# Kernel optimization log

Hardware: AMD Instinct MI355X
Metric: run time of the kernel (lower is better)

The kernel has to match this reference:

```python
import jax, jax.numpy as jnp
import numpy as np

N, E, F, H, C, G = 50000, 600000, 128, 128, 10, 500
NUM_GIN = 3
BN_EPS = 1e-5


def _bn(x, gamma, beta):
    # BatchNorm1d in training mode: batch statistics over node/graph dim
    m = jnp.mean(x, axis=0)
    v = jnp.mean((x - m) ** 2, axis=0)
    return (x - m) * jax.lax.rsqrt(v + BN_EPS) * gamma + beta


def setup_inputs() -> dict:
    key = jax.random.key(0)
    ks = jax.random.split(key, 16)
    s = 1.0 / np.sqrt(H)
    inp = {
        "x": jax.random.normal(ks[0], (N, F), dtype=jnp.float32),
        "edge_index": jax.random.randint(ks[1], (2, E), 0, N),
        "batch": jnp.sort(jax.random.randint(ks[2], (N,), 0, G)),
        # bn_feat
        "gamma_feat": jnp.ones((F,), jnp.float32),
        "beta_feat": jnp.full((F,), 1e-4, jnp.float32),
        # conv_feat (GCNConv gfn=True -> pure linear)
        "W_feat": jax.random.uniform(ks[3], (F, H), jnp.float32, -s, s),
        "b_feat": jnp.zeros((H,), jnp.float32),
        # GIN conv MLPs, stacked over 3 layers
        "gin_W1": jax.random.uniform(ks[4], (NUM_GIN, H, H), jnp.float32, -s, s),
        "gin_b1": jnp.zeros((NUM_GIN, H), jnp.float32),
        "gin_gamma": jnp.ones((NUM_GIN, H), jnp.float32),
        "gin_beta": jnp.full((NUM_GIN, H), 1e-4, jnp.float32),
        "gin_W2": jax.random.uniform(ks[5], (NUM_GIN, H, H), jnp.float32, -s, s),
        "gin_b2": jnp.zeros((NUM_GIN, H), jnp.float32),
        # one FC block (num_fc_layers=2 -> 1 bn+lin)
        "gamma_fc": jnp.ones((H,), jnp.float32),
        "beta_fc": jnp.full((H,), 1e-4, jnp.float32),
        "W_fc": jax.random.uniform(ks[6], (H, H), jnp.float32, -s, s),
        "b_fc": jnp.zeros((H,), jnp.float32),
        # bn_hidden + classifier
        "gamma_h": jnp.ones((H,), jnp.float32),
        "beta_h": jnp.full((H,), 1e-4, jnp.float32),
        "W_cls": jax.random.uniform(ks[7], (H, C), jnp.float32, -s, s),
        "b_cls": jnp.zeros((C,), jnp.float32),
    }
    return inp


def reference(x, gamma_feat, beta_feat, W_feat, b_feat,
              gin_W1, gin_b1, gin_gamma, gin_beta, gin_W2, gin_b2,
              gamma_fc, beta_fc, W_fc, b_fc,
              gamma_h, beta_h, W_cls, b_cls,
              edge_index, batch):
    src, dst = edge_index[0], edge_index[1]
    h = _bn(x, gamma_feat, beta_feat)
    h = jax.nn.relu(h @ W_feat + b_feat)  # GCNConv gfn=True == Linear
    for i in range(NUM_GIN):
        # GIN aggregation: (1+eps)*x + sum_{j->i} x_j, eps=0
        agg = jnp.zeros_like(h).at[dst].add(h[src])
        z = h + agg
        z = jax.nn.relu(_bn(z @ gin_W1[i] + gin_b1[i], gin_gamma[i], gin_beta[i]))
        h = jax.nn.relu(z @ gin_W2[i] + gin_b2[i])
    g = jax.ops.segment_sum(h, batch, num_segments=G)  # global_add_pool -> [G,H]
    g = jax.nn.relu(_bn(g, gamma_fc, beta_fc) @ W_fc + b_fc)
    g = _bn(g, gamma_h, beta_h)
    logits = g @ W_cls + b_cls
    return jax.nn.log_softmax(logits, axis=-1)
```

## Files before the change

kernel.cpp:

```cpp
#include <hip/hip_runtime.h>
#include <math.h>

#define N_NODES 50000
#define N_EDGES 600000
#define HDIM 128
#define NCLS 10
#define NGRAPH 500
#define BN_EPS 1e-5f
#define SCAN_BLOCKS 196

__global__ void colstats_kernel(const float* __restrict__ X, int M, float* __restrict__ stats) {
    int col = threadIdx.x & 127;
    int sub = threadIdx.x >> 7;
    float s = 0.f, sq = 0.f;
    for (int r = blockIdx.x * 2 + sub; r < M; r += gridDim.x * 2) {
        float v = X[(size_t)r * HDIM + col];
        s += v; sq += v * v;
    }
    atomicAdd(&stats[col], s);
    atomicAdd(&stats[HDIM + col], sq);
}

__global__ void hist_kernel(const int* __restrict__ ei, int* __restrict__ counts) {
    int e = blockIdx.x * 256 + threadIdx.x;
    if (e < N_EDGES) atomicAdd(&counts[ei[N_EDGES + e]], 1);
}

__global__ __launch_bounds__(256) void scan1_kernel(const int* __restrict__ counts,
                                                    int* __restrict__ partial,
                                                    int* __restrict__ blockSums) {
    __shared__ int tmp[256];
    int tid = threadIdx.x;
    int i = blockIdx.x * 256 + tid;
    int v = (i < N_NODES) ? counts[i] : 0;
    tmp[tid] = v;
    __syncthreads();
#pragma unroll
    for (int off = 1; off < 256; off <<= 1) {
        int t = (tid >= off) ? tmp[tid - off] : 0;
        __syncthreads();
        tmp[tid] += t;
        __syncthreads();
    }
    if (i < N_NODES) partial[i] = tmp[tid] - v;
    if (tid == 255) blockSums[blockIdx.x] = tmp[255];
}

__global__ __launch_bounds__(256) void scan2_kernel(const int* __restrict__ blockSums,
                                                    int* __restrict__ blockBase) {
    __shared__ int tmp[256];
    int tid = threadIdx.x;
    int v = (tid < SCAN_BLOCKS) ? blockSums[tid] : 0;
    tmp[tid] = v;
    __syncthreads();
#pragma unroll
    for (int off = 1; off < 256; off <<= 1) {
        int t = (tid >= off) ? tmp[tid - off] : 0;
        __syncthreads();
        tmp[tid] += t;
        __syncthreads();
    }
    if (tid < SCAN_BLOCKS) blockBase[tid] = tmp[tid] - v;
}

__global__ __launch_bounds__(256) void scan3_kernel(const int* __restrict__ partial,
                                                    const int* __restrict__ blockBase,
                                                    int* __restrict__ offsets,
                                                    int* __restrict__ cursor) {
    int i = blockIdx.x * 256 + threadIdx.x;
    if (i < N_NODES) {
        int o = partial[i] + blockBase[blockIdx.x];
        offsets[i] = o;
        cursor[i] = o;
    }
    if (i == 0) offsets[N_NODES] = N_EDGES;
}

__global__ void fill_kernel(const int* __restrict__ ei, int* __restrict__ cursor, int* __restrict__ csr) {
    int e = blockIdx.x * 256 + threadIdx.x;
    if (e < N_EDGES) {
        int d = ei[N_EDGES + e];
        int pos = atomicAdd(&cursor[d], 1);
        csr[pos] = ei[e];
    }
}

__global__ __launch_bounds__(256) void agg_kernel(const float* __restrict__ h,
                                                  const int* __restrict__ offsets,
                                                  const int* __restrict__ csr,
                                                  float* __restrict__ z) {
    int node = (blockIdx.x * 256 + threadIdx.x) >> 6;
    int lane = threadIdx.x & 63;
    if (node >= N_NODES) return;
    int c0 = lane * 2;
    int beg = offsets[node], end = offsets[node + 1];
    const float2 self = *(const float2*)&h[(size_t)node * HDIM + c0];
    float ax = self.x, ay = self.y;
    for (int j = beg; j < end; j += 64) {
        int cnt = min(64, end - j);
        int sl = (j + lane < end) ? csr[j + lane] : 0;
        int t = 0;
        for (; t + 4 <= cnt; t += 4) {
            int s0 = __shfl(sl, t, 64);
            int s1 = __shfl(sl, t + 1, 64);
            int s2 = __shfl(sl, t + 2, 64);
            int s3 = __shfl(sl, t + 3, 64);
            float2 v0 = *(const float2*)&h[(size_t)s0 * HDIM + c0];
            float2 v1 = *(const float2*)&h[(size_t)s1 * HDIM + c0];
            float2 v2 = *(const float2*)&h[(size_t)s2 * HDIM + c0];
            float2 v3 = *(const float2*)&h[(size_t)s3 * HDIM + c0];
            ax += v0.x + v1.x + v2.x + v3.x;
            ay += v0.y + v1.y + v2.y + v3.y;
        }
        for (; t < cnt; t++) {
            int s = __shfl(sl, t, 64);
            float2 hv = *(const float2*)&h[(size_t)s * HDIM + c0];
            ax += hv.x; ay += hv.y;
        }
    }
    float2 o; o.x = ax; o.y = ay;
    *(float2*)&z[(size_t)node * HDIM + c0] = o;
}

__global__ __launch_bounds__(128) void segsum2_kernel(const float* __restrict__ h,
                                                      const int* __restrict__ batch,
                                                      float* __restrict__ g) {
    int b = blockIdx.x;
    int tid = threadIdx.x;
    __shared__ int bounds[2];
    if (tid < 2) {
        int target = b + tid;
        int lo = 0, hi = N_NODES;
        while (lo < hi) {
            int mid = (lo + hi) >> 1;
            if (batch[mid] < target) lo = mid + 1; else hi = mid;
        }
        bounds[tid] = lo;
    }
    __syncthreads();
    int beg = bounds[0], end = bounds[1];
    float s = 0.f;
    for (int r = beg; r < end; r++) s += h[(size_t)r * HDIM + tid];
    g[b * HDIM + tid] = s;
}

template <bool PRE_A, bool PRE_B, bool RELU, bool STATS>
__global__ __launch_bounds__(256, 3) void gemm_bn(const float* A, const float* __restrict__ B,
                                                  const float* __restrict__ bias, float* C, int M,
                                                  const float* __restrict__ statsPre,
                                                  const float* __restrict__ gammaPre,
                                                  const float* __restrict__ betaPre,
                                                  float invCnt, float* __restrict__ statsOut) {
    __shared__ float At[64][65];
    __shared__ float Bs[64][128];
    __shared__ float aPre[128], bPre[128];

    const int tid = threadIdx.x;
    const int tx = tid & 15, ty = tid >> 4;
    const int r0 = blockIdx.x * 64;

    if (PRE_A || PRE_B) {
        if (tid < 128) {
            float m = statsPre[tid] * invCnt;
            float v = statsPre[128 + tid] * invCnt - m * m;
            float a = gammaPre[tid] * rsqrtf(v + BN_EPS);
            aPre[tid] = a;
            bPre[tid] = betaPre[tid] - m * a;
        }
        __syncthreads();
    }

    float acc[4][8];
#pragma unroll
    for (int i = 0; i < 4; i++)
#pragma unroll
        for (int j = 0; j < 8; j++) acc[i][j] = 0.f;

    float biasEff[8];
#pragma unroll
    for (int j = 0; j < 8; j++) biasEff[j] = bias[8 * tx + j];
    if (PRE_B) {
        for (int k = 0; k < 128; k++) {
            float bb = bPre[k];
            const float* Brow = B + (size_t)k * HDIM + 8 * tx;
#pragma unroll
            for (int j = 0; j < 8; j++) biasEff[j] = fmaf(bb, Brow[j], biasEff[j]);
        }
    }

    for (int kc = 0; kc < 128; kc += 64) {
#pragma unroll
        for (int i = 0; i < 4; i++) {
            int f4 = tid + i * 256;
            int row = f4 >> 4;
            int kg = f4 & 15;
            int grow = r0 + row;
            float4 av;
            if (grow < M) av = *(const float4*)(A + (size_t)grow * HDIM + kc + kg * 4);
            else av = make_float4(0.f, 0.f, 0.f, 0.f);
            if (PRE_A) {
                int kb = kc + kg * 4;
                av.x = fmaxf(fmaf(av.x, aPre[kb + 0], bPre[kb + 0]), 0.f);
                av.y = fmaxf(fmaf(av.y, aPre[kb + 1], bPre[kb + 1]), 0.f);
                av.z = fmaxf(fmaf(av.z, aPre[kb + 2], bPre[kb + 2]), 0.f);
                av.w = fmaxf(fmaf(av.w, aPre[kb + 3], bPre[kb + 3]), 0.f);
            }
            At[kg * 4 + 0][row] = av.x;
            At[kg * 4 + 1][row] = av.y;
            At[kg * 4 + 2][row] = av.z;
            At[kg * 4 + 3][row] = av.w;
        }
#pragma unroll
        for (int i = 0; i < 8; i++) {
            int f4 = tid + i * 256;
            int krow = f4 >> 5;
            int cg = f4 & 31;
            float4 bv = *(const float4*)(B + (size_t)(kc + krow) * HDIM + cg * 4);
            if (PRE_B) {
                float s = aPre[kc + krow];
                bv.x *= s; bv.y *= s; bv.z *= s; bv.w *= s;
            }
            *(float4*)&Bs[krow][cg * 4] = bv;
        }
        __syncthreads();
#pragma unroll 8
        for (int k = 0; k < 64; k++) {
            float av[4];
            av[0] = At[k][ty];
            av[1] = At[k][ty + 16];
            av[2] = At[k][ty + 32];
            av[3] = At[k][ty + 48];
            const float4 b0 = *(const float4*)&Bs[k][8 * tx];
            const float4 b1 = *(const float4*)&Bs[k][8 * tx + 4];
            float bv[8] = {b0.x, b0.y, b0.z, b0.w, b1.x, b1.y, b1.z, b1.w};
#pragma unroll
            for (int i = 0; i < 4; i++)
#pragma unroll
                for (int j = 0; j < 8; j++) acc[i][j] = fmaf(av[i], bv[j], acc[i][j]);
        }
        __syncthreads();
    }

    float s[8], sq[8];
    if (STATS) {
#pragma unroll
        for (int j = 0; j < 8; j++) { s[j] = 0.f; sq[j] = 0.f; }
    }
#pragma unroll
    for (int i = 0; i < 4; i++) {
        int grow = r0 + ty + 16 * i;
        if (grow < M) {
            float v[8];
#pragma unroll
            for (int j = 0; j < 8; j++) {
                v[j] = acc[i][j] + biasEff[j];
                if (RELU) v[j] = fmaxf(v[j], 0.f);
                if (STATS) { s[j] += v[j]; sq[j] += v[j] * v[j]; }
            }
            float4 o0 = make_float4(v[0], v[1], v[2], v[3]);
            float4 o1 = make_float4(v[4], v[5], v[6], v[7]);
            *(float4*)(C + (size_t)grow * HDIM + 8 * tx) = o0;
            *(float4*)(C + (size_t)grow * HDIM + 8 * tx + 4) = o1;
        }
    }
    if (STATS) {
        float* red = &At[0][0];
#pragma unroll
        for (int j = 0; j < 8; j++) {
            red[ty * 128 + 8 * tx + j] = s[j];
            red[2048 + ty * 128 + 8 * tx + j] = sq[j];
        }
        __syncthreads();
        if (tid < 128) {
            float t = 0.f;
#pragma unroll
            for (int u = 0; u < 16; u++) t += red[u * 128 + tid];
            atomicAdd(&statsOut[tid], t);
        } else {
            int col = tid - 128;
            float t = 0.f;
#pragma unroll
            for (int u = 0; u < 16; u++) t += red[2048 + u * 128 + col];
            atomicAdd(&statsOut[128 + col], t);
        }
    }
}

__global__ __launch_bounds__(256) void head_kernel(const float* __restrict__ g2,
                                                   const float* __restrict__ stats,
                                                   const float* __restrict__ gamma,
                                                   const float* __restrict__ beta,
                                                   const float* __restrict__ Wc,
                                                   const float* __restrict__ bc,
                                                   float* __restrict__ out, float invCnt) {
    __shared__ float Wf[HDIM * NCLS];
    __shared__ float bf[NCLS];
    __shared__ float aP[HDIM], bP[HDIM];
    const int tid = threadIdx.x;
    if (tid < HDIM) {
        float m = stats[tid] * invCnt;
        float v = stats[HDIM + tid] * invCnt - m * m;
        float a = gamma[tid] * rsqrtf(v + BN_EPS);
        aP[tid] = a;
        bP[tid] = beta[tid] - m * a;
    }
    __syncthreads();
    for (int idx = tid; idx < HDIM * NCLS; idx += 256) {
        int k = idx / NCLS;
        Wf[idx] = aP[k] * Wc[idx];
    }
    if (tid < NCLS) {
        float sv = bc[tid];
        for (int k = 0; k < HDIM; k++) sv = fmaf(bP[k], Wc[k * NCLS + tid], sv);
        bf[tid] = sv;
    }
    __syncthreads();
    int row = blockIdx.x * 256 + tid;
    if (row >= NGRAPH) return;
    float l[NCLS];
#pragma unroll
    for (int c = 0; c < NCLS; c++) l[c] = bf[c];
    for (int k = 0; k < HDIM; k++) {
        float gv = g2[row * HDIM + k];
#pragma unroll
        for (int c = 0; c < NCLS; c++) l[c] = fmaf(gv, Wf[k * NCLS + c], l[c]);
    }
    float mx = l[0];
#pragma unroll
    for (int c = 1; c < NCLS; c++) mx = fmaxf(mx, l[c]);
    float se = 0.f;
#pragma unroll
    for (int c = 0; c < NCLS; c++) se += expf(l[c] - mx);
    float lse = mx + logf(se);
#pragma unroll
    for (int c = 0; c < NCLS; c++) out[row * NCLS + c] = l[c] - lse;
}

extern "C" void kernel_launch(void* const* d_in, const int* in_sizes, int n_in,
                              void* d_out, int out_size, void* d_ws, size_t ws_size,
                              hipStream_t stream) {
    const float* x          = (const float*)d_in[0];
    const int*   ei         = (const int*)d_in[1];
    const int*   batch      = (const int*)d_in[2];
    const float* gamma_feat = (const float*)d_in[3];
    const float* beta_feat  = (const float*)d_in[4];
    const float* W_feat     = (const float*)d_in[5];
    const float* b_feat     = (const float*)d_in[6];
    const float* gin_W1     = (const float*)d_in[7];
    const float* gin_b1     = (const float*)d_in[8];
    const float* gin_gamma  = (const float*)d_in[9];
    const float* gin_beta   = (const float*)d_in[10];
    const float* gin_W2     = (const float*)d_in[11];
    const float* gin_b2     = (const float*)d_in[12];
    const float* gamma_fc   = (const float*)d_in[13];
    const float* beta_fc    = (const float*)d_in[14];
    const float* W_fc       = (const float*)d_in[15];
    const float* b_fc       = (const float*)d_in[16];
    const float* gamma_h    = (const float*)d_in[17];
    const float* beta_h     = (const float*)d_in[18];
    const float* W_cls      = (const float*)d_in[19];
    const float* b_cls      = (const float*)d_in[20];
    float* out = (float*)d_out;

    float* ws = (float*)d_ws;
    size_t off = 0;
    float* h  = ws + off; off += (size_t)N_NODES * HDIM;
    float* zy = ws + off; off += (size_t)N_NODES * HDIM;
    float* g2 = ws + off; off += NGRAPH * HDIM;
    float* g  = ws + off; off += NGRAPH * HDIM;
    size_t zstart = off;
    float* stats = ws + off; off += 256 * 6;
    int* counts = (int*)(ws + off); off += N_NODES;
    size_t zbytes = (off - zstart) * sizeof(float);
    int* offsets   = (int*)(ws + off); off += N_NODES + 1;
    int* cursor    = (int*)(ws + off); off += N_NODES;
    int* csr       = (int*)(ws + off); off += N_EDGES;
    int* partial   = (int*)(ws + off); off += N_NODES;
    int* blockSums = (int*)(ws + off); off += 256;
    int* blockBase = (int*)(ws + off); off += 256;

    float* statsX  = stats;
    float* statsY0 = stats + 256;
    float* statsY1 = stats + 512;
    float* statsY2 = stats + 768;
    float* statsYa[3] = {statsY0, statsY1, statsY2};
    float* statsG  = stats + 1024;
    float* statsG2 = stats + 1280;

    hipMemsetAsync(stats, 0, zbytes, stream);

    const float invN = 1.f / (float)N_NODES;
    const float invG = 1.f / (float)NGRAPH;
    const int gblocks = (N_NODES + 63) / 64;
    const int eblocks = (N_EDGES + 255) / 256;
    const int nwaves  = (N_NODES * 64 + 255) / 256;

    colstats_kernel<<<256, 256, 0, stream>>>(x, N_NODES, statsX);
    hist_kernel<<<eblocks, 256, 0, stream>>>(ei, counts);
    scan1_kernel<<<SCAN_BLOCKS, 256, 0, stream>>>(counts, partial, blockSums);
    scan2_kernel<<<1, 256, 0, stream>>>(blockSums, blockBase);
    scan3_kernel<<<SCAN_BLOCKS, 256, 0, stream>>>(partial, blockBase, offsets, cursor);
    fill_kernel<<<eblocks, 256, 0, stream>>>(ei, cursor, csr);

    gemm_bn<false, true, true, false><<<gblocks, 256, 0, stream>>>(
        x, W_feat, b_feat, h, N_NODES, statsX, gamma_feat, beta_feat, invN, nullptr);

    for (int i = 0; i < 3; i++) {
        agg_kernel<<<nwaves, 256, 0, stream>>>(h, offsets, csr, zy);
        gemm_bn<false, false, false, true><<<gblocks, 256, 0, stream>>>(
            zy, gin_W1 + i * HDIM * HDIM, gin_b1 + i * HDIM, zy, N_NODES,
            nullptr, nullptr, nullptr, invN, statsYa[i]);
        gemm_bn<true, false, true, false><<<gblocks, 256, 0, stream>>>(
            zy, gin_W2 + i * HDIM * HDIM, gin_b2 + i * HDIM, h, N_NODES,
            statsYa[i], gin_gamma + i * HDIM, gin_beta + i * HDIM, invN, nullptr);
    }

    segsum2_kernel<<<NGRAPH, 128, 0, stream>>>(h, batch, g);
    colstats_kernel<<<8, 256, 0, stream>>>(g, NGRAPH, statsG);
    gemm_bn<false, true, true, true><<<(NGRAPH + 63) / 64, 256, 0, stream>>>(
        g, W_fc, b_fc, g2, NGRAPH, statsG, gamma_fc, beta_fc, invG, statsG2);
    head_kernel<<<2, 256, 0, stream>>>(g2, statsG2, gamma_h, beta_h, W_cls, b_cls, out, invG);
}
```

Measured before the change: 737.4 us.

## Move node GEMMs to bf16x3 split-precision MFMA with pretransposed weights

Replaces the FP32 shared-memory GEMM kernels for the feature layer and the six GIN linear layers with an MFMA kernel. Each fp32 operand is split into a bf16 high part and a bf16 low part, and three bf16 MFMA products are summed to stay close to fp32 accuracy. Weights are split and transposed once by small prep kernels. The feature-layer batch norm is folded into the weights and bias, and the GIN batch norm plus ReLU is applied while loading A. This is meant to move the matmul work from SIMT FP32 onto the matrix cores, in exchange for extra split arithmetic and direct global loads of A and B with no LDS tiling.

```diff
diff --git a/kernel.cpp b/kernel.cpp
--- a/kernel.cpp
+++ b/kernel.cpp
@@ -8,6 +8,9 @@
 #define NGRAPH 500
 #define BN_EPS 1e-5f
 #define SCAN_BLOCKS 196
+
+typedef short bf16x8 __attribute__((ext_vector_type(8)));
+typedef float f32x4 __attribute__((ext_vector_type(4)));
 
 __global__ void colstats_kernel(const float* __restrict__ X, int M, float* __restrict__ stats) {
     int col = threadIdx.x & 127;
@@ -144,6 +147,176 @@
     g[b * HDIM + tid] = s;
 }
 
+__device__ inline void dekker_split(float v, unsigned short& hi, unsigned short& lo) {
+    unsigned u = __float_as_uint(v);
+    hi = (unsigned short)(u >> 16);
+    float flo = v - __uint_as_float(u & 0xffff0000u);
+    lo = (unsigned short)(__float_as_uint(flo) >> 16);
+}
+
+__global__ __launch_bounds__(256) void prep_w(const float* __restrict__ W1,
+                                              const float* __restrict__ W2,
+                                              unsigned short* __restrict__ wh,
+                                              unsigned short* __restrict__ wl) {
+    int m = blockIdx.x;
+    const float* src = (m < 3) ? (W1 + m * HDIM * HDIM) : (W2 + (m - 3) * HDIM * HDIM);
+    unsigned short* dh = wh + m * HDIM * HDIM;
+    unsigned short* dl = wl + m * HDIM * HDIM;
+    for (int i = threadIdx.x; i < HDIM * HDIM; i += 256) {
+        int n = i >> 7, k = i & 127;
+        float v = src[k * HDIM + n];
+        unsigned short h16, l16;
+        dekker_split(v, h16, l16);
+        dh[i] = h16; dl[i] = l16;
+    }
+}
+
+__global__ __launch_bounds__(256) void prep_feat(const float* __restrict__ W,
+                                                 const float* __restrict__ bfeat,
+                                                 const float* __restrict__ stats,
+                                                 const float* __restrict__ gamma,
+                                                 const float* __restrict__ beta,
+                                                 float invCnt,
+                                                 unsigned short* __restrict__ dh,
+                                                 unsigned short* __restrict__ dl,
+                                                 float* __restrict__ biasF) {
+    __shared__ float aP[HDIM], bP[HDIM];
+    int tid = threadIdx.x;
+    if (tid < HDIM) {
+        float m = stats[tid] * invCnt;
+        float v = stats[HDIM + tid] * invCnt - m * m;
+        float a = gamma[tid] * rsqrtf(v + BN_EPS);
+        aP[tid] = a;
+        bP[tid] = beta[tid] - m * a;
+    }
+    __syncthreads();
+    for (int i = tid; i < HDIM * HDIM; i += 256) {
+        int n = i >> 7, k = i & 127;
+        float v = aP[k] * W[k * HDIM + n];
+        unsigned short h16, l16;
+        dekker_split(v, h16, l16);
+        dh[i] = h16; dl[i] = l16;
+    }
+    if (tid < HDIM) {
+        float acc = bfeat[tid];
+        for (int k = 0; k < HDIM; k++) acc = fmaf(bP[k], W[k * HDIM + tid], acc);
+        biasF[tid] = acc;
+    }
+}
+
+template <int MODE>
+__global__ __launch_bounds__(256, 2) void mfma_gemm(const float* __restrict__ A,
+                                                    const unsigned short* __restrict__ Bh,
+                                                    const unsigned short* __restrict__ Bl,
+                                                    const float* __restrict__ bias,
+                                                    float* __restrict__ C, int M,
+                                                    const float* __restrict__ statsPre,
+                                                    const float* __restrict__ gammaPre,
+                                                    const float* __restrict__ betaPre,
+                                                    float invCnt,
+                                                    float* __restrict__ statsOut) {
+    const int tid = threadIdx.x;
+    const int w = tid >> 6, l = tid & 63;
+    const int q = l >> 4, c16 = l & 15;
+    const int rb = blockIdx.x * 128 + w * 32;
+
+    int rowA[2];
+#pragma unroll
+    for (int rt = 0; rt < 2; rt++) rowA[rt] = min(rb + rt * 16 + c16, M - 1);
+
+    float bs[8];
+#pragma unroll
+    for (int c = 0; c < 8; c++) bs[c] = bias[c * 16 + c16];
+
+    f32x4 acc[2][8];
+#pragma unroll
+    for (int rt = 0; rt < 2; rt++)
+#pragma unroll
+        for (int c = 0; c < 8; c++) acc[rt][c] = (f32x4){0.f, 0.f, 0.f, 0.f};
+
+#pragma unroll
+    for (int s = 0; s < 4; s++) {
+        const int k0 = s * 32 + q * 8;
+        float aK[8], bK[8];
+        if (MODE == 2) {
+#pragma unroll
+            for (int j = 0; j < 8; j++) {
+                int k = k0 + j;
+                float m = statsPre[k] * invCnt;
+                float var = statsPre[HDIM + k] * invCnt - m * m;
+                float a = gammaPre[k] * rsqrtf(var + BN_EPS);
+                aK[j] = a;
+                bK[j] = betaPre[k] - m * a;
+            }
+        }
+        bf16x8 ah[2], al[2];
+#pragma unroll
+        for (int rt = 0; rt < 2; rt++) {
+            const float* ap = A + (size_t)rowA[rt] * HDIM + k0;
+            float4 v0 = *(const float4*)ap;
+            float4 v1 = *(const float4*)(ap + 4);
+            float vv[8] = {v0.x, v0.y, v0.z, v0.w, v1.x, v1.y, v1.z, v1.w};
+#pragma unroll
+            for (int j = 0; j < 8; j++) {
+                float v = vv[j];
+                if (MODE == 2) v = fmaxf(fmaf(v, aK[j], bK[j]), 0.f);
+                unsigned u = __float_as_uint(v);
+                ah[rt][j] = (short)(u >> 16);
+                float flo = v - __uint_as_float(u & 0xffff0000u);
+                al[rt][j] = (short)(__float_as_uint(flo) >> 16);
+            }
+        }
+#pragma unroll
+        for (int c = 0; c < 8; c++) {
+            const size_t bo = (size_t)(c * 16 + c16) * HDIM + k0;
+            bf16x8 bh = *(const bf16x8*)(Bh + bo);
+            bf16x8 bl = *(const bf16x8*)(Bl + bo);
+#pragma unroll
+            for (int rt = 0; rt < 2; rt++) {
+                acc[rt][c] = __builtin_amdgcn_mfma_f32_16x16x32_bf16(ah[rt], bh, acc[rt][c], 0, 0, 0);
+                acc[rt][c] = __builtin_amdgcn_mfma_f32_16x16x32_bf16(al[rt], bh, acc[rt][c], 0, 0, 0);
+                acc[rt][c] = __builtin_amdgcn_mfma_f32_16x16x32_bf16(ah[rt], bl, acc[rt][c], 0, 0, 0);
+            }
+        }
+    }
+
+    float ssum[8], ssq[8];
+    if (MODE == 1) {
+#pragma unroll
+        for (int c = 0; c < 8; c++) { ssum[c] = 0.f; ssq[c] = 0.f; }
+    }
+#pragma unroll
+    for (int rt = 0; rt < 2; rt++) {
+#pragma unroll
+        for (int reg = 0; reg < 4; reg++) {
+            int row = rb + rt * 16 + q * 4 + reg;
+            if (row < M) {
+                float* cp = C + (size_t)row * HDIM + c16;
+#pragma unroll
+                for (int c = 0; c < 8; c++) {
+                    float v = acc[rt][c][reg] + bs[c];
+                    if (MODE != 1) v = fmaxf(v, 0.f);
+                    cp[c * 16] = v;
+                    if (MODE == 1) { ssum[c] += v; ssq[c] += v * v; }
+                }
+            }
+        }
+    }
+    if (MODE == 1) {
+#pragma unroll
+        for (int c = 0; c < 8; c++) {
+            float s2 = ssum[c] + __shfl_xor(ssum[c], 16, 64);
+            float s4 = s2 + __shfl_xor(s2, 32, 64);
+            float t2 = ssq[c] + __shfl_xor(ssq[c], 16, 64);
+            float t4 = t2 + __shfl_xor(t2, 32, 64);
+            if (q == 0) {
+                atomicAdd(&statsOut[c * 16 + c16], s4);
+                atomicAdd(&statsOut[HDIM + c * 16 + c16], t4);
+            }
+        }
+    }
+}
+
 template <bool PRE_A, bool PRE_B, bool RELU, bool STATS>
 __global__ __launch_bounds__(256, 3) void gemm_bn(const float* A, const float* __restrict__ B,
                                                   const float* __restrict__ bias, float* C, int M,
@@ -378,12 +551,13 @@
     int* partial   = (int*)(ws + off); off += N_NODES;
     int* blockSums = (int*)(ws + off); off += 256;
     int* blockBase = (int*)(ws + off); off += 256;
+    off = (off + 3) & ~(size_t)3;
+    unsigned short* wt_hi = (unsigned short*)(ws + off); off += 7 * HDIM * HDIM / 2;
+    unsigned short* wt_lo = (unsigned short*)(ws + off); off += 7 * HDIM * HDIM / 2;
+    float* biasF = ws + off; off += HDIM;
 
     float* statsX  = stats;
-    float* statsY0 = stats + 256;
-    float* statsY1 = stats + 512;
-    float* statsY2 = stats + 768;
-    float* statsYa[3] = {statsY0, statsY1, statsY2};
+    float* statsYa[3] = {stats + 256, stats + 512, stats + 768};
     float* statsG  = stats + 1024;
     float* statsG2 = stats + 1280;
 
@@ -391,28 +565,32 @@
 
     const float invN = 1.f / (float)N_NODES;
     const float invG = 1.f / (float)NGRAPH;
-    const int gblocks = (N_NODES + 63) / 64;
     const int eblocks = (N_EDGES + 255) / 256;
     const int nwaves  = (N_NODES * 64 + 255) / 256;
-
+    const int mblocks = (N_NODES + 127) / 128;
+
+    prep_w<<<6, 256, 0, stream>>>(gin_W1, gin_W2, wt_hi, wt_lo);
     colstats_kernel<<<256, 256, 0, stream>>>(x, N_NODES, statsX);
     hist_kernel<<<eblocks, 256, 0, stream>>>(ei, counts);
     scan1_kernel<<<SCAN_BLOCKS, 256, 0, stream>>>(counts, partial, blockSums);
     scan2_kernel<<<1, 256, 0, stream>>>(blockSums, blockBase);
     scan3_kernel<<<SCAN_BLOCKS, 256, 0, stream>>>(partial, blockBase, offsets, cursor);
     fill_kernel<<<eblocks, 256, 0, stream>>>(ei, cursor, csr);
-
-    gemm_bn<false, true, true, false><<<gblocks, 256, 0, stream>>>(
-        x, W_feat, b_feat, h, N_NODES, statsX, gamma_feat, beta_feat, invN, nullptr);
+    prep_feat<<<1, 256, 0, stream>>>(W_feat, b_feat, statsX, gamma_feat, beta_feat, invN,
+                                     wt_hi + 6 * HDIM * HDIM, wt_lo + 6 * HDIM * HDIM, biasF);
+
+    mfma_gemm<0><<<mblocks, 256, 0, stream>>>(
+        x, wt_hi + 6 * HDIM * HDIM, wt_lo + 6 * HDIM * HDIM, biasF, h, N_NODES,
+        nullptr, nullptr, nullptr, invN, nullptr);
 
     for (int i = 0; i < 3; i++) {
         agg_kernel<<<nwaves, 256, 0, stream>>>(h, offsets, csr, zy);
-        gemm_bn<false, false, false, true><<<gblocks, 256, 0, stream>>>(
-            zy, gin_W1 + i * HDIM * HDIM, gin_b1 + i * HDIM, zy, N_NODES,
-            nullptr, nullptr, nullptr, invN, statsYa[i]);
-        gemm_bn<true, false, true, false><<<gblocks, 256, 0, stream>>>(
-            zy, gin_W2 + i * HDIM * HDIM, gin_b2 + i * HDIM, h, N_NODES,
-            statsYa[i], gin_gamma + i * HDIM, gin_beta + i * HDIM, invN, nullptr);
+        mfma_gemm<1><<<mblocks, 256, 0, stream>>>(
+            zy, wt_hi + i * HDIM * HDIM, wt_lo + i * HDIM * HDIM, gin_b1 + i * HDIM,
+            zy, N_NODES, nullptr, nullptr, nullptr, invN, statsYa[i]);
+        mfma_gemm<2><<<mblocks, 256, 0, stream>>>(
+            zy, wt_hi + (3 + i) * HDIM * HDIM, wt_lo + (3 + i) * HDIM * HDIM, gin_b2 + i * HDIM,
+            h, N_NODES, statsYa[i], gin_gamma + i * HDIM, gin_beta + i * HDIM, invN, nullptr);
     }
 
     segsum2_kernel<<<NGRAPH, 128, 0, stream>>>(h, batch, g);
```

New measurement: 709.3 us. 3.8% less time.
